# Kernel tuning notes

Measured on AMD Instinct MI355X. Metric: run time of the kernel, lower is better.

The kernel has to match this reference:

```python
import jax, jax.numpy as jnp
import numpy as np

HEAD_DIM = 128

def _rope(t, cos, sin):
    # t: [B,S,Hx,HD]; cos/sin: [S,HD//2] -> broadcast [1,S,1,HD//2]
    tr = t.reshape(t.shape[:-1] + (-1, 2))
    t_r, t_i = tr[..., 0], tr[..., 1]
    c = cos[None, :, None, :]
    s = sin[None, :, None, :]
    o_r = t_r * c - t_i * s
    o_i = t_r * s + t_i * c
    return jnp.stack([o_r, o_i], axis=-1).reshape(t.shape)

def setup_inputs() -> dict:
    key = jax.random.key(0)
    ks = jax.random.split(key, 8)
    B, S, D = 2, 2048, 4096
    H, KVH, HD = 32, 8, HEAD_DIM
    x = jax.random.normal(ks[0], (B, S, D), jnp.float32)
    # realistic RoPE frequencies
    inv_freq = 1.0 / (10000.0 ** (np.arange(0, HD, 2, dtype=np.float32) / HD))
    t = np.arange(S, dtype=np.float32)
    ang = np.outer(t, inv_freq)  # [S, HD//2]
    freqs_cos = jnp.asarray(np.cos(ang))
    freqs_sin = jnp.asarray(np.sin(ang))
    positions = jnp.arange(S, dtype=jnp.int32)
    # causal additive mask [S,S]
    mask = jnp.where(jnp.tril(jnp.ones((S, S), bool)), 0.0, -1e9).astype(jnp.float32)
    sc = lambda fan: 1.0 / np.sqrt(fan)
    wq = jax.random.normal(ks[1], (H * HD, D), jnp.float32) * sc(D)
    wk = jax.random.normal(ks[2], (KVH * HD, D), jnp.float32) * sc(D)
    wv = jax.random.normal(ks[3], (KVH * HD, D), jnp.float32) * sc(D)
    wo = jax.random.normal(ks[4], (D, H * HD), jnp.float32) * sc(H * HD)
    return {"x": x, "freqs_cos": freqs_cos, "freqs_sin": freqs_sin,
            "positions": positions, "mask": mask,
            "wq": wq, "wk": wk, "wv": wv, "wo": wo}

def reference(x, freqs_cos, freqs_sin, positions, mask, wq, wk, wv, wo):
    B, S, D = x.shape
    HD = freqs_cos.shape[-1] * 2
    H = wq.shape[0] // HD
    KVH = wk.shape[0] // HD
    repeats = H // KVH
    scale = HD ** -0.5
    xq = (x @ wq.T).reshape(B, S, H, HD)
    xk = (x @ wk.T).reshape(B, S, KVH, HD)
    xv = (x @ wv.T).reshape(B, S, KVH, HD)
    xq = _rope(xq, freqs_cos, freqs_sin)
    xk = _rope(xk, freqs_cos, freqs_sin)
    # GQA broadcast (prefill branch: positions.shape[0] > 1)
    key = jnp.repeat(xk, repeats, axis=2)  # [B,S,H,HD]
    val = jnp.repeat(xv, repeats, axis=2)
    scores = jnp.einsum('bqhd,bkhd->bhqk', xq, key) * scale
    scores = scores + mask[None, None, :, :]
    probs = jax.nn.softmax(scores.astype(jnp.float32), axis=-1).astype(xq.dtype)
    out = jnp.einsum('bhqk,bkhd->bqhd', probs, val).reshape(B, S, H * HD)
    return out @ wo.T
```

## Files before the change

### kernel.cpp

```cpp
#include <hip/hip_runtime.h>
#include <math.h>

typedef unsigned short u16;
typedef short bf16x8 __attribute__((ext_vector_type(8)));
typedef float f32x4 __attribute__((ext_vector_type(4)));
typedef u16 u16x2 __attribute__((ext_vector_type(2)));
typedef u16 u16x4 __attribute__((ext_vector_type(4)));
typedef u16 u16x8 __attribute__((ext_vector_type(8)));

#define MFMA16(a, b, c) __builtin_amdgcn_mfma_f32_16x16x32_bf16(a, b, c, 0, 0, 0)

#define GLL16(g, l)                                                  \
    __builtin_amdgcn_global_load_lds(                                \
        (__attribute__((address_space(1))) void*)(g),                \
        (__attribute__((address_space(3))) void*)(l), 16, 0, 0)

__device__ __forceinline__ float bf2f(u16 u) {
    union { unsigned int i; float f; } v;
    v.i = ((unsigned int)u) << 16;
    return v.f;
}
__device__ __forceinline__ u16 f2bf(float f) {
    union { float f; unsigned int i; } v;
    v.f = f;
    unsigned int r = (v.i + 0x7FFFu + ((v.i >> 16) & 1u)) >> 16;
    return (u16)r;
}
__device__ __forceinline__ u16x4 cvt4(f32x4 v) {
    u16x4 r;
#pragma unroll
    for (int j = 0; j < 4; ++j) r[j] = f2bf(v[j]);
    return r;
}

__global__ __launch_bounds__(256)
void cvt_bf16(const float* __restrict__ in, u16* __restrict__ out, int n8) {
    int i = blockIdx.x * 256 + threadIdx.x;
    const int stride = gridDim.x * 256;
    for (; i < n8; i += stride) {
        f32x4 a = ((const f32x4*)in)[2 * i];
        f32x4 b = ((const f32x4*)in)[2 * i + 1];
        u16x8 o;
#pragma unroll
        for (int j = 0; j < 4; ++j) { o[j] = f2bf(a[j]); o[4 + j] = f2bf(b[j]); }
        ((u16x8*)out)[i] = o;
    }
}

template<bool OUT_F32, bool OUT_TRANS>
__global__ __launch_bounds__(256, 2)
void gemm_bb(const u16* __restrict__ A, const u16* __restrict__ B,
             void* __restrict__ Cv, int M, int N, int K) {
    __shared__ __align__(16) u16 As[128 * 32];
    __shared__ __align__(16) u16 Bs[128 * 32];
    const int tid  = threadIdx.x;
    const int wave = tid >> 6, lane = tid & 63;
    const int lr = lane & 15, quad = lane >> 4;
    const int m0 = blockIdx.y * 128, n0 = blockIdx.x * 128;
    const int wr = (wave >> 1) * 64, wc = (wave & 1) * 64;

    const int srow = tid >> 2;
    const int scol = (tid & 3) * 8;
    const u16* ag = A + (size_t)(m0 + srow) * K + scol;
    const u16* bg = B + (size_t)(n0 + srow) * K + scol;
    const size_t rowskip = (size_t)64 * K;
    u16* asl = As + wave * 512;
    u16* bsl = Bs + wave * 512;

    f32x4 acc[4][4] = {};

    for (int k0 = 0; k0 < K; k0 += 32) {
        __syncthreads();
        GLL16(ag + k0,           asl);
        GLL16(ag + rowskip + k0, asl + 2048);
        GLL16(bg + k0,           bsl);
        GLL16(bg + rowskip + k0, bsl + 2048);
        __syncthreads();

        bf16x8 af[4], bfv[4];
#pragma unroll
        for (int i = 0; i < 4; ++i)
            af[i] = *(const bf16x8*)(As + (wr + i * 16 + lr) * 32 + quad * 8);
#pragma unroll
        for (int j = 0; j < 4; ++j)
            bfv[j] = *(const bf16x8*)(Bs + (wc + j * 16 + lr) * 32 + quad * 8);
#pragma unroll
        for (int i = 0; i < 4; ++i)
#pragma unroll
            for (int j = 0; j < 4; ++j)
                acc[i][j] = MFMA16(af[i], bfv[j], acc[i][j]);
    }

    if (OUT_TRANS) {
#pragma unroll
        for (int i = 0; i < 4; ++i) {
            int row0 = m0 + wr + i * 16 + quad * 4;
#pragma unroll
            for (int j = 0; j < 4; ++j) {
                int col = n0 + wc + j * 16 + lr;
                *(u16x4*)((u16*)Cv + (size_t)col * M + row0) = cvt4(acc[i][j]);
            }
        }
        return;
    }
#pragma unroll
    for (int i = 0; i < 4; ++i) {
#pragma unroll
        for (int r = 0; r < 4; ++r) {
            int row = m0 + wr + i * 16 + quad * 4 + r;
#pragma unroll
            for (int j = 0; j < 4; ++j) {
                int col = n0 + wc + j * 16 + lr;
                if (OUT_F32)
                    ((float*)Cv)[(size_t)row * N + col] = acc[i][j][r];
                else
                    ((u16*)Cv)[(size_t)row * N + col] = f2bf(acc[i][j][r]);
            }
        }
    }
}

template<bool A_BF16, bool OUT_F32>
__global__ __launch_bounds__(256, 2)
void gemm_bt(const void* __restrict__ Av, const float* __restrict__ W,
             void* __restrict__ Cv, int M, int N, int K) {
    __shared__ __align__(16) u16 As[128 * 40];
    __shared__ __align__(16) u16 Bs[128 * 40];
    const int tid  = threadIdx.x;
    const int wave = tid >> 6, lane = tid & 63;
    const int lr = lane & 15, quad = lane >> 4;
    const int m0 = blockIdx.y * 128, n0 = blockIdx.x * 128;
    const int wr = (wave >> 1) * 64, wc = (wave & 1) * 64;

    const int r8 = tid >> 3;
    const int c4 = (tid & 7) * 4;
    const int r4 = tid >> 2;
    const int c8 = (tid & 3) * 8;

    f32x4 acc[4][4] = {};

    for (int k0 = 0; k0 < K; k0 += 32) {
        f32x4 wreg[4];
#pragma unroll
        for (int rep = 0; rep < 4; ++rep)
            wreg[rep] = *(const f32x4*)(W + (size_t)(n0 + rep * 32 + r8) * K + k0 + c4);
        f32x4 aregf[4];
        u16x8 aregb[2];
        if (A_BF16) {
#pragma unroll
            for (int rep = 0; rep < 2; ++rep)
                aregb[rep] = *(const u16x8*)((const u16*)Av + (size_t)(m0 + rep * 64 + r4) * K + k0 + c8);
        } else {
#pragma unroll
            for (int rep = 0; rep < 4; ++rep)
                aregf[rep] = *(const f32x4*)((const float*)Av + (size_t)(m0 + rep * 32 + r8) * K + k0 + c4);
        }
        __syncthreads();
#pragma unroll
        for (int rep = 0; rep < 4; ++rep)
            *(u16x4*)(Bs + (rep * 32 + r8) * 40 + c4) = cvt4(wreg[rep]);
        if (A_BF16) {
#pragma unroll
            for (int rep = 0; rep < 2; ++rep)
                *(u16x8*)(As + (rep * 64 + r4) * 40 + c8) = aregb[rep];
        } else {
#pragma unroll
            for (int rep = 0; rep < 4; ++rep)
                *(u16x4*)(As + (rep * 32 + r8) * 40 + c4) = cvt4(aregf[rep]);
        }
        __syncthreads();

        bf16x8 af[4], bfv[4];
#pragma unroll
        for (int i = 0; i < 4; ++i)
            af[i] = *(const bf16x8*)(As + (wr + i * 16 + lr) * 40 + quad * 8);
#pragma unroll
        for (int j = 0; j < 4; ++j)
            bfv[j] = *(const bf16x8*)(Bs + (wc + j * 16 + lr) * 40 + quad * 8);
#pragma unroll
        for (int i = 0; i < 4; ++i)
#pragma unroll
            for (int j = 0; j < 4; ++j)
                acc[i][j] = MFMA16(af[i], bfv[j], acc[i][j]);
    }

#pragma unroll
    for (int i = 0; i < 4; ++i) {
#pragma unroll
        for (int r = 0; r < 4; ++r) {
            int row = m0 + wr + i * 16 + quad * 4 + r;
#pragma unroll
            for (int j = 0; j < 4; ++j) {
                int col = n0 + wc + j * 16 + lr;
                if (OUT_F32)
                    ((float*)Cv)[(size_t)row * N + col] = acc[i][j][r];
                else
                    ((u16*)Cv)[(size_t)row * N + col] = f2bf(acc[i][j][r]);
            }
        }
    }
}

__global__ void rope_k(u16* __restrict__ q, u16* __restrict__ kk) {
    const int QP = 2 * 2048 * 32 * 64;
    const int KP = 2 * 2048 * 8 * 64;
    int idx = blockIdx.x * 256 + threadIdx.x;
    u16* ptr;
    int s, i;
    if (idx < QP) {
        i = idx & 63;
        int h = (idx >> 6) & 31;
        int m = idx >> 11;
        s = m & 2047;
        ptr = q + (size_t)m * 4096 + h * 128 + 2 * i;
    } else {
        idx -= QP;
        if (idx >= KP) return;
        i = idx & 63;
        int h = (idx >> 6) & 7;
        int m = idx >> 9;
        s = m & 2047;
        ptr = kk + (size_t)m * 1024 + h * 128 + 2 * i;
    }
    float inv = expf(-9.210340371976184f * (float)(2 * i) * (1.0f / 128.0f));
    float ang = (float)s * inv;
    float sn = sinf(ang);
    float c  = cosf(ang);
    u16x2 v = *(u16x2*)ptr;
    float tr = bf2f(v[0]), ti = bf2f(v[1]);
    u16x2 o;
    o[0] = f2bf(tr * c - ti * sn);
    o[1] = f2bf(tr * sn + ti * c);
    *(u16x2*)ptr = o;
}

__global__ __launch_bounds__(256, 2)
void flash_attn(const u16* Q, const u16* __restrict__ K,
                const u16* __restrict__ Vt_g, u16* O) {
    __shared__ __align__(16) u16 Ks[2][64 * 128];
    __shared__ __align__(16) u16 Vs[2][128 * 64];
    __shared__ __align__(16) u16 Ps[4 * 16 * 72];
    const float scale = 0.08838834764831845f;
    const int tid  = threadIdx.x;
    const int wave = tid >> 6, lane = tid & 63;
    const int lr = lane & 15, quad = lane >> 4;
    const int p = blockIdx.x;
    const int h = blockIdx.y, b = blockIdx.z;
    const int hk  = h >> 2;
    const int bS  = b * 2048;

    const int ktr = tid >> 4;
    const int kd  = ((tid & 15) ^ (ktr & 7)) * 8;
    const u16* kg = K + (size_t)(bS + ktr) * 1024 + hk * 128 + kd;
    const int vdr = tid >> 3;
    const int vk0 = ((tid & 7) ^ (vdr & 7)) * 8;
    const u16* vg = Vt_g + (size_t)(hk * 128 + vdr) * 4096 + bS + vk0;
    u16* kl0 = &Ks[0][0] + wave * 512;
    u16* vl0 = &Vs[0][0] + wave * 512;

    auto STAGE = [&](int t, int buf) {
        const u16* kgk = kg + (size_t)(t * 64) * 1024;
        const u16* vgk = vg + t * 64;
        u16* klb = kl0 + buf * 8192;
        u16* vlb = vl0 + buf * 8192;
#pragma unroll
        for (int it = 0; it < 4; ++it) {
            GLL16(kgk + (size_t)(it * 16) * 1024, klb + it * 2048);
            GLL16(vgk + (size_t)(it * 32) * 4096, vlb + it * 2048);
        }
    };

    bf16x8 onesf;
#pragma unroll
    for (int j = 0; j < 8; ++j) onesf[j] = (short)0x3F80;

    for (int pass = 0; pass < 2; ++pass) {
        const int qb  = pass ? p : 31 - p;
        const int qg0 = qb * 64;

        bf16x8 qf[4];
        {
            const u16* qp = Q + (size_t)(bS + qg0 + wave * 16 + lr) * 4096 + h * 128 + quad * 8;
#pragma unroll
            for (int kc = 0; kc < 4; ++kc) qf[kc] = *(const bf16x8*)(qp + kc * 32);
        }

        f32x4 o[8] = {};
        f32x4 rsacc = {};
        float mrow[4] = {-1e30f, -1e30f, -1e30f, -1e30f};

        STAGE(0, 0);

        for (int kt = 0; kt <= qb; ++kt) {
            const int cur = kt & 1;
            if (kt < qb) {
                STAGE(kt + 1, cur ^ 1);
                asm volatile("s_waitcnt vmcnt(8)" ::: "memory");
            } else {
                asm volatile("s_waitcnt vmcnt(0)" ::: "memory");
            }
            __builtin_amdgcn_s_barrier();

            const u16* Ksb = &Ks[cur][0];
            const u16* Vsb = &Vs[cur][0];

            f32x4 sc[4] = {};
            __builtin_amdgcn_s_setprio(1);
#pragma unroll
            for (int t = 0; t < 4; ++t) {
                int key = t * 16 + lr;
#pragma unroll
                for (int kc = 0; kc < 4; ++kc) {
                    bf16x8 kf = *(const bf16x8*)(Ksb + key * 128 + (((kc * 4 + quad) ^ (lr & 7)) << 3));
                    sc[t] = MFMA16(qf[kc], kf, sc[t]);
                }
            }
            __builtin_amdgcn_s_setprio(0);

            const bool diag = (kt == qb);
#pragma unroll
            for (int t = 0; t < 4; ++t) {
#pragma unroll
                for (int r = 0; r < 4; ++r) {
                    float sv = sc[t][r] * scale;
                    if (diag) {
                        int key = kt * 64 + t * 16 + lr;
                        int qg  = qg0 + wave * 16 + quad * 4 + r;
                        if (key > qg) sv = -1e30f;
                    }
                    sc[t][r] = sv;
                }
            }

            float pmax[4];
#pragma unroll
            for (int r = 0; r < 4; ++r)
                pmax[r] = fmaxf(fmaxf(sc[0][r], sc[1][r]), fmaxf(sc[2][r], sc[3][r]));
            bool ok = true;
#pragma unroll
            for (int r = 0; r < 4; ++r) ok = ok && (pmax[r] - mrow[r] <= 8.0f);
            if (!__all(ok)) {
                float alpha[4];
#pragma unroll
                for (int r = 0; r < 4; ++r) {
                    float mx = pmax[r];
#pragma unroll
                    for (int d = 1; d < 16; d <<= 1) mx = fmaxf(mx, __shfl_xor(mx, d, 64));
                    float mn = fmaxf(mrow[r], mx);
                    alpha[r] = __expf(mrow[r] - mn);
                    mrow[r]  = mn;
                }
#pragma unroll
                for (int nt = 0; nt < 8; ++nt)
#pragma unroll
                    for (int r = 0; r < 4; ++r) o[nt][r] *= alpha[r];
#pragma unroll
                for (int r = 0; r < 4; ++r) rsacc[r] *= alpha[r];
            }
#pragma unroll
            for (int t = 0; t < 4; ++t)
#pragma unroll
                for (int r = 0; r < 4; ++r)
                    sc[t][r] = __expf(sc[t][r] - mrow[r]);

            u16* Pw = Ps + wave * (16 * 72);
#pragma unroll
            for (int t = 0; t < 4; ++t)
#pragma unroll
                for (int r = 0; r < 4; ++r)
                    Pw[(quad * 4 + r) * 72 + t * 16 + lr] = f2bf(sc[t][r]);

            bf16x8 pa[2];
#pragma unroll
            for (int c = 0; c < 2; ++c)
                pa[c] = *(const bf16x8*)(Pw + lr * 72 + c * 32 + quad * 8);

            __builtin_amdgcn_s_setprio(1);
            rsacc = MFMA16(pa[0], onesf, rsacc);
            rsacc = MFMA16(pa[1], onesf, rsacc);
#pragma unroll
            for (int nt = 0; nt < 8; ++nt) {
#pragma unroll
                for (int c = 0; c < 2; ++c) {
                    bf16x8 bv = *(const bf16x8*)(Vsb + (nt * 16 + lr) * 64 + (((c * 4 + quad) ^ (lr & 7)) << 3));
                    o[nt] = MFMA16(pa[c], bv, o[nt]);
                }
            }
            __builtin_amdgcn_s_setprio(0);

            __builtin_amdgcn_s_barrier();
        }

        float inv[4];
#pragma unroll
        for (int r = 0; r < 4; ++r) inv[r] = 1.0f / rsacc[r];
#pragma unroll
        for (int nt = 0; nt < 8; ++nt) {
#pragma unroll
            for (int r = 0; r < 4; ++r) {
                int tok = bS + qg0 + wave * 16 + quad * 4 + r;
                int col = h * 128 + nt * 16 + lr;
                O[(size_t)tok * 4096 + col] = f2bf(o[nt][r] * inv[r]);
            }
        }
    }
}

extern "C" void kernel_launch(void* const* d_in, const int* in_sizes, int n_in,
                              void* d_out, int out_size, void* d_ws, size_t ws_size,
                              hipStream_t stream) {
    const float* x  = (const float*)d_in[0];
    const float* wq = (const float*)d_in[5];
    const float* wk = (const float*)d_in[6];
    const float* wv = (const float*)d_in[7];
    const float* wo = (const float*)d_in[8];
    float* out = (float*)d_out;

    u16* qws  = (u16*)d_ws;
    u16* xb   = (u16*)d_out;
    u16* wqb  = xb + (32u << 20) / 2;
    u16* wkb  = wqb;
    u16* wvb  = wkb + (8u << 20) / 2;
    u16* kws  = wvb + (8u << 20) / 2;
    u16* vtws = kws + (8u << 20) / 2;

    dim3 blk(256);
    cvt_bf16<<<dim3(2048), blk, 0, stream>>>(x,  xb,  2097152);
    cvt_bf16<<<dim3(2048), blk, 0, stream>>>(wq, wqb, 2097152);
    gemm_bb<false, false><<<dim3(32, 32), blk, 0, stream>>>(xb, wqb, qws, 4096, 4096, 4096);
    cvt_bf16<<<dim3(1024), blk, 0, stream>>>(wk, wkb, 524288);
    cvt_bf16<<<dim3(1024), blk, 0, stream>>>(wv, wvb, 524288);
    gemm_bb<false, false><<<dim3(8, 32), blk, 0, stream>>>(xb, wkb, kws, 4096, 1024, 4096);
    gemm_bb<false, true ><<<dim3(8, 32), blk, 0, stream>>>(xb, wvb, vtws, 4096, 1024, 4096);
    rope_k<<<dim3(40960), blk, 0, stream>>>(qws, kws);
    flash_attn<<<dim3(16, 32, 2), blk, 0, stream>>>(qws, kws, vtws, qws);
    if (ws_size >= (size_t)(64u << 20)) {
        u16* wob = qws + (32u << 20) / 2;
        cvt_bf16<<<dim3(2048), blk, 0, stream>>>(wo, wob, 2097152);
        gemm_bb<true, false><<<dim3(32, 32), blk, 0, stream>>>(qws, wob, out, 4096, 4096, 4096);
    } else {
        gemm_bt<true, true><<<dim3(32, 32), blk, 0, stream>>>(qws, wo, out, 4096, 4096, 4096);
    }
}
```

Before: 850.9 us.

## Fuse RoPE into QKV GEMM epilogues and merge K and V projections

Removes the separate RoPE kernel and applies rotary embedding in the GEMM epilogue, using the provided cos/sin tables and a lane shuffle to fetch the paired element. The K and V projections become one GEMM over a concatenated weight buffer, with the V half written transposed. This saves one launch plus a full read-modify-write pass over Q and K, and gives the KV GEMM a larger grid. In exchange the epilogue gathers cos/sin values per element, and the workspace layout was changed to fit the combined weights.

Result: faster. 753.8 us (-11.4%).

```diff
diff --git a/kernel.cpp b/kernel.cpp
--- a/kernel.cpp
+++ b/kernel.cpp
@@ -47,10 +47,12 @@
     }
 }
 
-template<bool OUT_F32, bool OUT_TRANS>
+template<int MODE>
 __global__ __launch_bounds__(256, 2)
 void gemm_bb(const u16* __restrict__ A, const u16* __restrict__ B,
-             void* __restrict__ Cv, int M, int N, int K) {
+             void* __restrict__ Cv, u16* __restrict__ Ct,
+             const float* __restrict__ fc, const float* __restrict__ fs,
+             int M, int N, int K) {
     __shared__ __align__(16) u16 As[128 * 32];
     __shared__ __align__(16) u16 Bs[128 * 32];
     const int tid  = threadIdx.x;
@@ -91,30 +93,31 @@
                 acc[i][j] = MFMA16(af[i], bfv[j], acc[i][j]);
     }
 
-    if (OUT_TRANS) {
-#pragma unroll
-        for (int i = 0; i < 4; ++i) {
-            int row0 = m0 + wr + i * 16 + quad * 4;
-#pragma unroll
-            for (int j = 0; j < 4; ++j) {
-                int col = n0 + wc + j * 16 + lr;
-                *(u16x4*)((u16*)Cv + (size_t)col * M + row0) = cvt4(acc[i][j]);
-            }
-        }
-        return;
-    }
 #pragma unroll
     for (int i = 0; i < 4; ++i) {
-#pragma unroll
-        for (int r = 0; r < 4; ++r) {
-            int row = m0 + wr + i * 16 + quad * 4 + r;
-#pragma unroll
-            for (int j = 0; j < 4; ++j) {
-                int col = n0 + wc + j * 16 + lr;
-                if (OUT_F32)
-                    ((float*)Cv)[(size_t)row * N + col] = acc[i][j][r];
-                else
-                    ((u16*)Cv)[(size_t)row * N + col] = f2bf(acc[i][j][r]);
+        const int row0 = m0 + wr + i * 16 + quad * 4;
+#pragma unroll
+        for (int j = 0; j < 4; ++j) {
+            const int col = n0 + wc + j * 16 + lr;
+            if (MODE == 1) {
+#pragma unroll
+                for (int r = 0; r < 4; ++r)
+                    ((float*)Cv)[(size_t)(row0 + r) * N + col] = acc[i][j][r];
+            } else if (MODE == 3 && col >= 1024) {
+                *(u16x4*)(Ct + (size_t)(col - 1024) * M + row0) = cvt4(acc[i][j]);
+            } else {
+                const int   ifq = (col >> 1) & 63;
+                const float sgn = (col & 1) ? 1.0f : -1.0f;
+                const int   ld  = (MODE == 3) ? 1024 : 4096;
+#pragma unroll
+                for (int r = 0; r < 4; ++r) {
+                    int tok = (row0 + r) & 2047;
+                    float c = fc[tok * 64 + ifq];
+                    float s = fs[tok * 64 + ifq];
+                    float v  = acc[i][j][r];
+                    float pv = __shfl_xor(v, 1, 64);
+                    ((u16*)Cv)[(size_t)(row0 + r) * ld + col] = f2bf(v * c + sgn * (pv * s));
+                }
             }
         }
     }
@@ -199,39 +202,6 @@
             }
         }
     }
-}
-
-__global__ void rope_k(u16* __restrict__ q, u16* __restrict__ kk) {
-    const int QP = 2 * 2048 * 32 * 64;
-    const int KP = 2 * 2048 * 8 * 64;
-    int idx = blockIdx.x * 256 + threadIdx.x;
-    u16* ptr;
-    int s, i;
-    if (idx < QP) {
-        i = idx & 63;
-        int h = (idx >> 6) & 31;
-        int m = idx >> 11;
-        s = m & 2047;
-        ptr = q + (size_t)m * 4096 + h * 128 + 2 * i;
-    } else {
-        idx -= QP;
-        if (idx >= KP) return;
-        i = idx & 63;
-        int h = (idx >> 6) & 7;
-        int m = idx >> 9;
-        s = m & 2047;
-        ptr = kk + (size_t)m * 1024 + h * 128 + 2 * i;
-    }
-    float inv = expf(-9.210340371976184f * (float)(2 * i) * (1.0f / 128.0f));
-    float ang = (float)s * inv;
-    float sn = sinf(ang);
-    float c  = cosf(ang);
-    u16x2 v = *(u16x2*)ptr;
-    float tr = bf2f(v[0]), ti = bf2f(v[1]);
-    u16x2 o;
-    o[0] = f2bf(tr * c - ti * sn);
-    o[1] = f2bf(tr * sn + ti * c);
-    *(u16x2*)ptr = o;
 }
 
 __global__ __launch_bounds__(256, 2)
@@ -410,6 +380,8 @@
                               void* d_out, int out_size, void* d_ws, size_t ws_size,
                               hipStream_t stream) {
     const float* x  = (const float*)d_in[0];
+    const float* fc = (const float*)d_in[1];
+    const float* fs = (const float*)d_in[2];
     const float* wq = (const float*)d_in[5];
     const float* wk = (const float*)d_in[6];
     const float* wv = (const float*)d_in[7];
@@ -418,27 +390,29 @@
 
     u16* qws  = (u16*)d_ws;
     u16* xb   = (u16*)d_out;
-    u16* wqb  = xb + (32u << 20) / 2;
-    u16* wkb  = wqb;
-    u16* wvb  = wkb + (8u << 20) / 2;
-    u16* kws  = wvb + (8u << 20) / 2;
-    u16* vtws = kws + (8u << 20) / 2;
+    u16* wqb  = xb + (size_t)32 * 524288;
+    u16* kws  = xb + (size_t)32 * 524288;
+    u16* vtws = xb + (size_t)40 * 524288;
+    u16* wkvb = xb + (size_t)48 * 524288;
 
     dim3 blk(256);
     cvt_bf16<<<dim3(2048), blk, 0, stream>>>(x,  xb,  2097152);
     cvt_bf16<<<dim3(2048), blk, 0, stream>>>(wq, wqb, 2097152);
-    gemm_bb<false, false><<<dim3(32, 32), blk, 0, stream>>>(xb, wqb, qws, 4096, 4096, 4096);
-    cvt_bf16<<<dim3(1024), blk, 0, stream>>>(wk, wkb, 524288);
-    cvt_bf16<<<dim3(1024), blk, 0, stream>>>(wv, wvb, 524288);
-    gemm_bb<false, false><<<dim3(8, 32), blk, 0, stream>>>(xb, wkb, kws, 4096, 1024, 4096);
-    gemm_bb<false, true ><<<dim3(8, 32), blk, 0, stream>>>(xb, wvb, vtws, 4096, 1024, 4096);
-    rope_k<<<dim3(40960), blk, 0, stream>>>(qws, kws);
+    gemm_bb<2><<<dim3(32, 32), blk, 0, stream>>>(xb, wqb, qws, nullptr, fc, fs,
+                                                 4096, 4096, 4096);
+    cvt_bf16<<<dim3(1024), blk, 0, stream>>>(wk, wkvb,                      524288);
+    cvt_bf16<<<dim3(1024), blk, 0, stream>>>(wv, wkvb + (size_t)8 * 524288, 524288);
+    gemm_bb<3><<<dim3(16, 32), blk, 0, stream>>>(xb, wkvb, kws, vtws, fc, fs,
+                                                 4096, 2048, 4096);
     flash_attn<<<dim3(16, 32, 2), blk, 0, stream>>>(qws, kws, vtws, qws);
     if (ws_size >= (size_t)(64u << 20)) {
-        u16* wob = qws + (32u << 20) / 2;
+        u16* wob = qws + (size_t)32 * 524288;
         cvt_bf16<<<dim3(2048), blk, 0, stream>>>(wo, wob, 2097152);
-        gemm_bb<true, false><<<dim3(32, 32), blk, 0, stream>>>(qws, wob, out, 4096, 4096, 4096);
+        gemm_bb<1><<<dim3(32, 32), blk, 0, stream>>>(qws, wob, out, nullptr,
+                                                     nullptr, nullptr,
+                                                     4096, 4096, 4096);
     } else {
-        gemm_bt<true, true><<<dim3(32, 32), blk, 0, stream>>>(qws, wo, out, 4096, 4096, 4096);
-    }
-}
+        gemm_bt<true, true><<<dim3(32, 32), blk, 0, stream>>>(qws, wo, out,
+                                                              4096, 4096, 4096);
+    }
+}
```
